# Optimization experiments

Measured on AMD Instinct MI355X. Metric: run time of the kernel, lower is better.

The kernel has to match this reference:

```python
import jax, jax.numpy as jnp
import numpy as np

RADIUS = 4
SIGMA_X = 5.0
SIGMA_I = 1.0


def gaussian_kernel3d():
    # norm.pdf(d)/norm.pdf(0) == exp(-d^2/2)
    r = RADIUS
    n = 2 * r + 1
    v = np.linspace(-r, r, n) ** 2
    xy, yz, zx = np.meshgrid(v, v, v)
    dist = (xy + yz + zx) / SIGMA_X
    k = np.exp(-0.5 * dist ** 2).astype(np.float32)  # (9,9,9)
    return jnp.asarray(k)


def setup_inputs() -> dict:
    key = jax.random.key(0)
    k1, k2 = jax.random.split(key)
    B, C, K, D, H, W = 2, 1, 5, 96, 96, 96
    inputs = jax.random.normal(k1, (B, C, D, H, W), jnp.float32)
    logits = jax.random.normal(k2, (B, K, D, H, W), jnp.float32)
    labels = jax.nn.softmax(logits, axis=1)  # class probabilities
    return {"inputs": inputs, "labels": labels}


def reference(inputs, labels):
    # inputs: [B,C,D,H,W] raw image; labels: [B,K,D,H,W] class probs
    K = labels.shape[1]
    kernel = gaussian_kernel3d()
    eps_m, eps_d = 1e-5, 1e-6

    # per-class, per-channel weighted mean: [B,K,C]
    num_mean = jnp.mean(inputs[:, None] * labels[:, :, None], axis=(3, 4, 5))
    den_mean = jnp.mean(labels, axis=(2, 3, 4))[..., None] + eps_m  # [B,K,1]
    class_mean = num_mean / den_mean  # [B,K,C]

    # diff: sum over channels of (x - mean)^2 -> [B,K,D,H,W]
    diff = jnp.sum((inputs[:, None] - class_mean[..., None, None, None]) ** 2, axis=2)
    weights = jnp.exp(-(diff ** 2) / (SIGMA_I ** 2))  # [B,K,D,H,W]

    # depthwise (per-class) 3D conv with the shared Gaussian kernel
    rhs = jnp.broadcast_to(kernel[None, None], (K, 1) + kernel.shape)  # [K,1,9,9,9]
    pad = [(RADIUS, RADIUS)] * 3

    def conv(x):  # x: [B,K,D,H,W]
        return jax.lax.conv_general_dilated(
            x, rhs, window_strides=(1, 1, 1), padding=pad,
            dimension_numbers=("NCDHW", "OIDHW", "NCDHW"),
            feature_group_count=K)

    numer = jnp.sum(labels * conv(labels * weights), axis=(0, 2, 3, 4))  # [K]
    denom = jnp.sum(labels * conv(weights), axis=(0, 2, 3, 4))  # [K]
    loss = jnp.sum(jnp.abs(numer / (denom + eps_d)))  # L1Loss vs zeros per class
    return jnp.asarray(K, inputs.dtype) - loss
```

## Files before the change

kernel.cpp:

```cpp
#include <hip/hip_runtime.h>
#include <math.h>

#define VOL (96*96*96)
#define KCLS 5
#define CZ 12
#define PSTR 64
#define PROWS 40
#define PSZ (PROWS*PSTR)
#define NS2 15

typedef __attribute__((ext_vector_type(8))) short bf16x8;
typedef __attribute__((ext_vector_type(4))) float f32x4;
typedef __attribute__((ext_vector_type(4))) unsigned short us4;

constexpr int S2VALS[NS2] = {0,1,2,4,5,8,9,10,13,16,17,18,20,25,32};
constexpr int MAP33[33] = {0,1,2,-1,3,4,-1,-1,5,6,7,-1,-1,8,-1,-1,
                           9,10,11,-1,12,-1,-1,-1,-1,13,-1,-1,-1,-1,-1,-1,14};

__device__ __forceinline__ unsigned short f2bf(float f) {
  unsigned u = __builtin_bit_cast(unsigned, f);
  u += 0x7fffu + ((u >> 16) & 1u);
  return (unsigned short)(u >> 16);
}


__global__ __launch_bounds__(256) void k_sums(const float* __restrict__ I,
                                              const float* __restrict__ L,
                                              double* __restrict__ ws) {
  const int b = blockIdx.y;
  const int base = blockIdx.x * 256 + threadIdx.x;
  const float4 iv = ((const float4*)(I + b * VOL))[base];
  float sL[KCLS], sIL[KCLS];
#pragma unroll
  for (int k = 0; k < KCLS; ++k) {
    const float4 lv = ((const float4*)(L + (b * KCLS + k) * VOL))[base];
    sL[k] = (lv.x + lv.y) + (lv.z + lv.w);
    sIL[k] = iv.x * lv.x + iv.y * lv.y + iv.z * lv.z + iv.w * lv.w;
  }
#pragma unroll
  for (int k = 0; k < KCLS; ++k) {
#pragma unroll
    for (int off = 32; off; off >>= 1) {
      sL[k] += __shfl_down(sL[k], off);
      sIL[k] += __shfl_down(sIL[k], off);
    }
  }
  __shared__ double red[4][2 * KCLS];
  const int wid = threadIdx.x >> 6;
  if ((threadIdx.x & 63) == 0) {
#pragma unroll
    for (int k = 0; k < KCLS; ++k) {
      red[wid][k] = (double)sL[k];
      red[wid][KCLS + k] = (double)sIL[k];
    }
  }
  __syncthreads();
  if (threadIdx.x < 2 * KCLS) {
    double v = red[0][threadIdx.x] + red[1][threadIdx.x] + red[2][threadIdx.x] + red[3][threadIdx.x];
    const int k = threadIdx.x % KCLS;
    const int which = threadIdx.x / KCLS;
    const int slot = blockIdx.x & 31;
    atomicAdd(&ws[32 + which * 320 + (b * KCLS + k) * 32 + slot], v);
  }
}

__global__ __launch_bounds__(256, 3) void k_conv(const float* __restrict__ I,
                                                 const float* __restrict__ L,
                                                 double* __restrict__ ws) {
  __shared__ __attribute__((aligned(16))) short Wp[2][PSZ];
  __shared__ __attribute__((aligned(16))) short LWp[2][PSZ];
  __shared__ double red[8];
  __shared__ float meanS;

  const int t = threadIdx.x;
  const int vol = blockIdx.z;
  const int kcl = vol % KCLS;
  const int b = vol / KCLS;
  const int x0 = (blockIdx.x % 3) * 32;
  const int y0 = (blockIdx.x / 3) * 32;
  const int z0 = blockIdx.y * CZ;

  const float* __restrict__ Ib = I + b * VOL;
  const float* __restrict__ Lb = L + vol * VOL;

  if (t < 32) {
    double a = ws[32 + vol * 32 + t];
    double c = ws[352 + vol * 32 + t];
#pragma unroll
    for (int off = 16; off; off >>= 1) {
      a += __shfl_down(a, off);
      c += __shfl_down(c, off);
    }
    if (t == 0) meanS = (float)(c / (a + 1e-5 * (double)VOL));
  }
  __syncthreads();
  const float mean = meanS;

  const int lane = t & 63;
  const int w = t >> 6;
  const int wx = w & 1, wy = w >> 1;
  const int nn = lane & 15, qq = lane >> 4;
  const int gyOut = y0 + 16 * wy + nn;
  const int gxOut = x0 + 16 * wx + 4 * qq;

  bf16x8 afr[NS2];
#pragma unroll
  for (int r = 0; r < NS2; ++r) {
    const float s2c = (float)S2VALS[r];
    bf16x8 v;
#pragma unroll
    for (int j = 0; j < 8; ++j) {
      const int dx = 8 * qq + j - nn;
      float val = 0.f;
      if (dx >= 0 && dx <= 8) {
        const float q = s2c + (float)((dx - 4) * (dx - 4));
        val = __expf(-0.02f * q * q);
      }
      v[j] = (short)f2bf(val);
    }
    afr[r] = v;
  }

  f32x4 accW[9], accL[9];
  const f32x4 zer = {0.f, 0.f, 0.f, 0.f};
#pragma unroll
  for (int i = 0; i < 9; ++i) { accW[i] = zer; accL[i] = zer; }
  float pN = 0.f, pD = 0.f;

  auto stagePlane = [&](int buf, int zp) {
#pragma unroll
    for (int ii = 0; ii < 2; ++ii) {
      const int qi = t + ii * 256;
      if (qi < 480) {
        const int row = qi / 12;
        const int q = qi - row * 12;
        const int xq = q * 4;
        const int gy = y0 - 4 + row, gx = x0 - 4 + xq;
        const bool ok = ((unsigned)gy < 96u) && ((unsigned)gx <= 92u);
        float4 iv = make_float4(0.f, 0.f, 0.f, 0.f);
        float4 lv = make_float4(0.f, 0.f, 0.f, 0.f);
        if (ok) {
          const int off = (zp * 96 + gy) * 96 + gx;
          iv = *(const float4*)(Ib + off);
          lv = *(const float4*)(Lb + off);
        }
        float d, w0, w1, w2, w3;
        d = iv.x - mean; d = d * d; w0 = ok ? __expf(-d * d) : 0.f;
        d = iv.y - mean; d = d * d; w1 = ok ? __expf(-d * d) : 0.f;
        d = iv.z - mean; d = d * d; w2 = ok ? __expf(-d * d) : 0.f;
        d = iv.w - mean; d = d * d; w3 = ok ? __expf(-d * d) : 0.f;
        us4 wv = { f2bf(w0), f2bf(w1), f2bf(w2), f2bf(w3) };
        us4 ov = { f2bf(lv.x * w0), f2bf(lv.y * w1), f2bf(lv.z * w2), f2bf(lv.w * w3) };
        const int c = q >> 1, o = (q & 1) << 2;
        const int a = row * PSTR + (((c ^ (row & 7)) << 3) + o);
        *(us4*)(&Wp[buf][a]) = wv;
        *(us4*)(&LWp[buf][a]) = ov;
      }
    }
  };

  auto computeEdge = [&](int buf, int iLo, int iHi) {
    const short* __restrict__ Wb = Wp[buf];
    const short* __restrict__ Lwb = LWp[buf];
    const int yb = 16 * wy + nn;
    const int csel = 2 * wx + qq;
    int boff = yb * PSTR + (((csel ^ (yb & 7))) << 3);
    bf16x8 bw = *(const bf16x8*)(Wb + boff);
    bf16x8 bl = *(const bf16x8*)(Lwb + boff);
#pragma unroll
    for (int dy = 0; dy < 9; ++dy) {
      bf16x8 nbw, nbl;
      if (dy < 8) {
        const int yrow = yb + dy + 1;
        const int nboff = yrow * PSTR + (((csel ^ (yrow & 7))) << 3);
        nbw = *(const bf16x8*)(Wb + nboff);
        nbl = *(const bf16x8*)(Lwb + nboff);
      }
      const int dy2c = (dy - 4) * (dy - 4);
#pragma unroll
      for (int i = 0; i < 9; ++i) {
        if (i >= iLo && i <= iHi) {
          const int da = (i < 4) ? (4 - i) : (i - 4);
          const int ri = MAP33[dy2c + da * da];
          accW[i] = __builtin_amdgcn_mfma_f32_16x16x32_bf16(afr[ri], bw, accW[i], 0, 0, 0);
          accL[i] = __builtin_amdgcn_mfma_f32_16x16x32_bf16(afr[ri], bl, accL[i], 0, 0, 0);
        }
      }
      bw = nbw; bl = nbl;
    }
  };

  const int zp0 = z0 - 4;
  const int zend = z0 + CZ + 4;
  if ((unsigned)zp0 <= 95u) stagePlane(0, zp0);
  __syncthreads();

  for (int zp = zp0; zp < zend; ++zp) {
    const int cur = (zp - zp0) & 1;
    const int zo = zp - 4;
    const bool lok = (zo >= z0) && (zo < z0 + CZ);
    float4 lab = make_float4(0.f, 0.f, 0.f, 0.f);
    if (lok) lab = *(const float4*)(Lb + (zo * 96 + gyOut) * 96 + gxOut);

    if ((unsigned)zp <= 95u) {
      int iLo = z0 - zo; if (iLo < 0) iLo = 0;
      int iHi = (z0 + CZ - 1) - zo; if (iHi > 8) iHi = 8;
      computeEdge(cur, iLo, iHi);
    }
    if (lok) {
      pN += accL[0].x * lab.x + accL[0].y * lab.y + accL[0].z * lab.z + accL[0].w * lab.w;
      pD += accW[0].x * lab.x + accW[0].y * lab.y + accW[0].z * lab.z + accW[0].w * lab.w;
    }
#pragma unroll
    for (int i = 0; i < 8; ++i) { accW[i] = accW[i + 1]; accL[i] = accL[i + 1]; }
    accW[8] = zer; accL[8] = zer;

    const int zn = zp + 1;
    if (zn < zend && (unsigned)zn <= 95u) stagePlane(cur ^ 1, zn);
    __syncthreads();
  }

#pragma unroll
  for (int off = 32; off; off >>= 1) {
    pN += __shfl_down(pN, off);
    pD += __shfl_down(pD, off);
  }
  if (lane == 0) { red[w] = (double)pN; red[4 + w] = (double)pD; }
  __syncthreads();
  if (t == 0) {
    const int slot = (blockIdx.x + blockIdx.y) & 15;
    atomicAdd(&ws[672 + kcl * 16 + slot], red[0] + red[1] + red[2] + red[3]);
    atomicAdd(&ws[752 + kcl * 16 + slot], red[4] + red[5] + red[6] + red[7]);
  }
}

__global__ void k_final(const double* __restrict__ ws, float* __restrict__ out) {
  __shared__ double acc[KCLS];
  const int t = threadIdx.x;
  if (t < KCLS) {
    double n = 0.0, d = 0.0;
#pragma unroll
    for (int s = 0; s < 16; ++s) {
      n += ws[672 + t * 16 + s];
      d += ws[752 + t * 16 + s];
    }
    acc[t] = fabs(n / (d + 1e-6));
  }
  __syncthreads();
  if (t == 0) {
    double loss = acc[0] + acc[1] + acc[2] + acc[3] + acc[4];
    out[0] = (float)(5.0 - loss);
  }
}

extern "C" void kernel_launch(void* const* d_in, const int* in_sizes, int n_in,
                              void* d_out, int out_size, void* d_ws, size_t ws_size,
                              hipStream_t stream) {
  (void)in_sizes; (void)n_in; (void)out_size; (void)ws_size;
  const float* I = (const float*)d_in[0];
  const float* L = (const float*)d_in[1];
  double* ws = (double*)d_ws;
  float* out = (float*)d_out;

  hipMemsetAsync(d_ws, 0, 832 * sizeof(double), stream);
  k_sums<<<dim3(864, 2, 1), 256, 0, stream>>>(I, L, ws);
  k_conv<<<dim3(9, 8, 10), 256, 0, stream>>>(I, L, ws);
  k_final<<<1, 64, 0, stream>>>(ws, out);
}
```

Measured before the change: 184.4 us.

## Use single-wave conv blocks, prune tiny Gaussian taps, fuse final reduction

The conv kernel now uses 64-thread blocks over 16x16 tiles, with one wave each. That lets it drop the per-plane __syncthreads and shrink the padded LDS planes. Kernel tap groups with squared y/z distance of 20 or more are removed from the MFMA loop, which skips small-weight contributions and introduces a small approximation. The z loop is clamped to valid planes, with a tail loop to drain the accumulators. The separate final kernel is replaced by a last-block-done atomic counter inside the conv kernel, saving a launch at the cost of extra atomics and fences.

```diff
diff --git a/kernel.cpp b/kernel.cpp
--- a/kernel.cpp
+++ b/kernel.cpp
@@ -4,18 +4,20 @@
 #define VOL (96*96*96)
 #define KCLS 5
 #define CZ 12
-#define PSTR 64
-#define PROWS 40
+#define PSTR 32
+#define PROWS 24
 #define PSZ (PROWS*PSTR)
-#define NS2 15
+#define NS2 12
+#define NQ 144
+#define NBLK 2880
 
 typedef __attribute__((ext_vector_type(8))) short bf16x8;
 typedef __attribute__((ext_vector_type(4))) float f32x4;
 typedef __attribute__((ext_vector_type(4))) unsigned short us4;
 
-constexpr int S2VALS[NS2] = {0,1,2,4,5,8,9,10,13,16,17,18,20,25,32};
+constexpr int S2VALS[NS2] = {0,1,2,4,5,8,9,10,13,16,17,18};
 constexpr int MAP33[33] = {0,1,2,-1,3,4,-1,-1,5,6,7,-1,-1,8,-1,-1,
-                           9,10,11,-1,12,-1,-1,-1,-1,13,-1,-1,-1,-1,-1,-1,14};
+                           9,10,11,-1,-1,-1,-1,-1,-1,-1,-1,-1,-1,-1,-1,-1,-1};
 
 __device__ __forceinline__ unsigned short f2bf(float f) {
   unsigned u = __builtin_bit_cast(unsigned, f);
@@ -64,44 +66,44 @@
   }
 }
 
-__global__ __launch_bounds__(256, 3) void k_conv(const float* __restrict__ I,
-                                                 const float* __restrict__ L,
-                                                 double* __restrict__ ws) {
+__global__ __launch_bounds__(64, 3) void k_conv(const float* __restrict__ I,
+                                                const float* __restrict__ L,
+                                                double* __restrict__ ws,
+                                                float* __restrict__ out) {
   __shared__ __attribute__((aligned(16))) short Wp[2][PSZ];
   __shared__ __attribute__((aligned(16))) short LWp[2][PSZ];
-  __shared__ double red[8];
-  __shared__ float meanS;
 
   const int t = threadIdx.x;
   const int vol = blockIdx.z;
   const int kcl = vol % KCLS;
   const int b = vol / KCLS;
-  const int x0 = (blockIdx.x % 3) * 32;
-  const int y0 = (blockIdx.x / 3) * 32;
+  const int x0 = (blockIdx.x % 6) * 16;
+  const int y0 = (blockIdx.x / 6) * 16;
   const int z0 = blockIdx.y * CZ;
 
   const float* __restrict__ Ib = I + b * VOL;
   const float* __restrict__ Lb = L + vol * VOL;
 
-  if (t < 32) {
-    double a = ws[32 + vol * 32 + t];
-    double c = ws[352 + vol * 32 + t];
-#pragma unroll
-    for (int off = 16; off; off >>= 1) {
-      a += __shfl_down(a, off);
-      c += __shfl_down(c, off);
-    }
-    if (t == 0) meanS = (float)(c / (a + 1e-5 * (double)VOL));
-  }
-  __syncthreads();
-  const float mean = meanS;
-
-  const int lane = t & 63;
-  const int w = t >> 6;
-  const int wx = w & 1, wy = w >> 1;
-  const int nn = lane & 15, qq = lane >> 4;
-  const int gyOut = y0 + 16 * wy + nn;
-  const int gxOut = x0 + 16 * wx + 4 * qq;
+  {
+    const bf16x8 z8 = {};
+#pragma unroll
+    for (int i = 0; i < 3; ++i) {
+      ((bf16x8*)Wp)[t + i * 64] = z8;
+      ((bf16x8*)LWp)[t + i * 64] = z8;
+    }
+  }
+
+  double a0 = ws[32 + vol * 32 + (t & 31)];
+  double c0 = ws[352 + vol * 32 + (t & 31)];
+#pragma unroll
+  for (int off = 1; off < 32; off <<= 1) {
+    a0 += __shfl_xor(a0, off);
+    c0 += __shfl_xor(c0, off);
+  }
+  const float mean = (float)(c0 / (a0 + 1e-5 * (double)VOL));
+
+  const int nn = t & 15, qq = t >> 4;
+  const int gyOut = y0 + nn, gxOut = x0 + 4 * qq;
 
   bf16x8 afr[NS2];
 #pragma unroll
@@ -129,11 +131,11 @@
 
   auto stagePlane = [&](int buf, int zp) {
 #pragma unroll
-    for (int ii = 0; ii < 2; ++ii) {
-      const int qi = t + ii * 256;
-      if (qi < 480) {
-        const int row = qi / 12;
-        const int q = qi - row * 12;
+    for (int ii = 0; ii < 3; ++ii) {
+      const int qi = t + ii * 64;
+      if (qi < NQ) {
+        const int row = qi / 6;
+        const int q = qi - row * 6;
         const int xq = q * 4;
         const int gy = y0 - 4 + row, gx = x0 - 4 + xq;
         const bool ok = ((unsigned)gy < 96u) && ((unsigned)gx <= 92u);
@@ -152,61 +154,60 @@
         us4 wv = { f2bf(w0), f2bf(w1), f2bf(w2), f2bf(w3) };
         us4 ov = { f2bf(lv.x * w0), f2bf(lv.y * w1), f2bf(lv.z * w2), f2bf(lv.w * w3) };
         const int c = q >> 1, o = (q & 1) << 2;
-        const int a = row * PSTR + (((c ^ (row & 7)) << 3) + o);
+        const int a = row * PSTR + ((c ^ (row & 3)) << 3) + o;
         *(us4*)(&Wp[buf][a]) = wv;
         *(us4*)(&LWp[buf][a]) = ov;
       }
     }
   };
 
-  auto computeEdge = [&](int buf, int iLo, int iHi) {
+  auto computeE = [&](int buf, int iLo, int iHi) {
     const short* __restrict__ Wb = Wp[buf];
     const short* __restrict__ Lwb = LWp[buf];
-    const int yb = 16 * wy + nn;
-    const int csel = 2 * wx + qq;
-    int boff = yb * PSTR + (((csel ^ (yb & 7))) << 3);
+    int boff = nn * PSTR + ((qq ^ (nn & 3)) << 3);
     bf16x8 bw = *(const bf16x8*)(Wb + boff);
     bf16x8 bl = *(const bf16x8*)(Lwb + boff);
 #pragma unroll
     for (int dy = 0; dy < 9; ++dy) {
       bf16x8 nbw, nbl;
       if (dy < 8) {
-        const int yrow = yb + dy + 1;
-        const int nboff = yrow * PSTR + (((csel ^ (yrow & 7))) << 3);
-        nbw = *(const bf16x8*)(Wb + nboff);
-        nbl = *(const bf16x8*)(Lwb + nboff);
+        const int r2 = nn + dy + 1;
+        const int nb = r2 * PSTR + ((qq ^ (r2 & 3)) << 3);
+        nbw = *(const bf16x8*)(Wb + nb);
+        nbl = *(const bf16x8*)(Lwb + nb);
       }
       const int dy2c = (dy - 4) * (dy - 4);
 #pragma unroll
       for (int i = 0; i < 9; ++i) {
-        if (i >= iLo && i <= iHi) {
-          const int da = (i < 4) ? (4 - i) : (i - 4);
-          const int ri = MAP33[dy2c + da * da];
-          accW[i] = __builtin_amdgcn_mfma_f32_16x16x32_bf16(afr[ri], bw, accW[i], 0, 0, 0);
-          accL[i] = __builtin_amdgcn_mfma_f32_16x16x32_bf16(afr[ri], bl, accL[i], 0, 0, 0);
+        const int da = (i < 4) ? (4 - i) : (i - 4);
+        const int ri = MAP33[dy2c + da * da];
+        if (ri >= 0) {
+          if (i >= iLo && i <= iHi) {
+            accW[i] = __builtin_amdgcn_mfma_f32_16x16x32_bf16(afr[ri], bw, accW[i], 0, 0, 0);
+            accL[i] = __builtin_amdgcn_mfma_f32_16x16x32_bf16(afr[ri], bl, accL[i], 0, 0, 0);
+          }
         }
       }
       bw = nbw; bl = nbl;
     }
   };
 
-  const int zp0 = z0 - 4;
-  const int zend = z0 + CZ + 4;
-  if ((unsigned)zp0 <= 95u) stagePlane(0, zp0);
-  __syncthreads();
-
-  for (int zp = zp0; zp < zend; ++zp) {
-    const int cur = (zp - zp0) & 1;
+  const int zlo = max(z0 - 4, 0);
+  const int zhi = min(z0 + CZ + 4, 96);
+
+  stagePlane(0, zlo);
+  for (int zp = zlo; zp < zhi; ++zp) {
+    const int cur = (zp - zlo) & 1;
+    const bool more = (zp + 1 < zhi);
     const int zo = zp - 4;
     const bool lok = (zo >= z0) && (zo < z0 + CZ);
     float4 lab = make_float4(0.f, 0.f, 0.f, 0.f);
     if (lok) lab = *(const float4*)(Lb + (zo * 96 + gyOut) * 96 + gxOut);
 
-    if ((unsigned)zp <= 95u) {
-      int iLo = z0 - zo; if (iLo < 0) iLo = 0;
-      int iHi = (z0 + CZ - 1) - zo; if (iHi > 8) iHi = 8;
-      computeEdge(cur, iLo, iHi);
-    }
+    int iLo = z0 - zo; if (iLo < 0) iLo = 0;
+    int iHi = (z0 + CZ - 1) - zo; if (iHi > 8) iHi = 8;
+    computeE(cur, iLo, iHi);
+
     if (lok) {
       pN += accL[0].x * lab.x + accL[0].y * lab.y + accL[0].z * lab.z + accL[0].w * lab.w;
       pD += accW[0].x * lab.x + accW[0].y * lab.y + accW[0].z * lab.z + accW[0].w * lab.w;
@@ -215,9 +216,15 @@
     for (int i = 0; i < 8; ++i) { accW[i] = accW[i + 1]; accL[i] = accL[i + 1]; }
     accW[8] = zer; accL[8] = zer;
 
-    const int zn = zp + 1;
-    if (zn < zend && (unsigned)zn <= 95u) stagePlane(cur ^ 1, zn);
-    __syncthreads();
+    if (more) stagePlane(cur ^ 1, zp + 1);
+  }
+
+  for (int zo = zhi - 4; zo < z0 + CZ; ++zo) {
+    const float4 lab = *(const float4*)(Lb + (zo * 96 + gyOut) * 96 + gxOut);
+    pN += accL[0].x * lab.x + accL[0].y * lab.y + accL[0].z * lab.z + accL[0].w * lab.w;
+    pD += accW[0].x * lab.x + accW[0].y * lab.y + accW[0].z * lab.z + accW[0].w * lab.w;
+#pragma unroll
+    for (int i = 0; i < 8; ++i) { accW[i] = accW[i + 1]; accL[i] = accL[i + 1]; }
   }
 
 #pragma unroll
@@ -225,31 +232,31 @@
     pN += __shfl_down(pN, off);
     pD += __shfl_down(pD, off);
   }
-  if (lane == 0) { red[w] = (double)pN; red[4 + w] = (double)pD; }
-  __syncthreads();
+  int lastf = 0;
   if (t == 0) {
     const int slot = (blockIdx.x + blockIdx.y) & 15;
-    atomicAdd(&ws[672 + kcl * 16 + slot], red[0] + red[1] + red[2] + red[3]);
-    atomicAdd(&ws[752 + kcl * 16 + slot], red[4] + red[5] + red[6] + red[7]);
-  }
-}
-
-__global__ void k_final(const double* __restrict__ ws, float* __restrict__ out) {
-  __shared__ double acc[KCLS];
-  const int t = threadIdx.x;
-  if (t < KCLS) {
-    double n = 0.0, d = 0.0;
-#pragma unroll
-    for (int s = 0; s < 16; ++s) {
-      n += ws[672 + t * 16 + s];
-      d += ws[752 + t * 16 + s];
-    }
-    acc[t] = fabs(n / (d + 1e-6));
-  }
-  __syncthreads();
-  if (t == 0) {
-    double loss = acc[0] + acc[1] + acc[2] + acc[3] + acc[4];
-    out[0] = (float)(5.0 - loss);
+    atomicAdd(&ws[672 + kcl * 16 + slot], (double)pN);
+    atomicAdd(&ws[752 + kcl * 16 + slot], (double)pD);
+    __threadfence();
+    lastf = (atomicAdd((int*)ws, 1) == NBLK - 1);
+  }
+  lastf = __shfl(lastf, 0);
+  if (lastf) {
+    __threadfence();
+    double v = 0.0;
+    if (t < KCLS) {
+      double n = 0.0, d = 0.0;
+#pragma unroll
+      for (int s = 0; s < 16; ++s) {
+        n += atomicAdd(&ws[672 + t * 16 + s], 0.0);
+        d += atomicAdd(&ws[752 + t * 16 + s], 0.0);
+      }
+      v = fabs(n / (d + 1e-6));
+    }
+    v += __shfl_down(v, 4);
+    v += __shfl_down(v, 2);
+    v += __shfl_down(v, 1);
+    if (t == 0) out[0] = (float)(5.0 - v);
   }
 }
 
@@ -264,6 +271,5 @@
 
   hipMemsetAsync(d_ws, 0, 832 * sizeof(double), stream);
   k_sums<<<dim3(864, 2, 1), 256, 0, stream>>>(I, L, ws);
-  k_conv<<<dim3(9, 8, 10), 256, 0, stream>>>(I, L, ws);
-  k_final<<<1, 64, 0, stream>>>(ws, out);
-}
+  k_conv<<<dim3(36, 8, 10), 64, 0, stream>>>(I, L, ws, out);
+}
```

Result: slower. 283.3 us (+53.6%).
